# Performance work log

Measured on AMD Instinct MI355X. Metric: run time of the kernel, lower is better.

The kernel has to match this reference:

```python
import jax, jax.numpy as jnp
import numpy as np

B, S, D_IN, D_OUT, H = 1, 4096, 1024, 1024, 16
HD = D_OUT // H


def setup_inputs() -> dict:
    key = jax.random.key(0)
    ks = jax.random.split(key, 6)
    sc = 0.02
    return {
        "x": jax.random.normal(ks[0], (B, S, D_IN), dtype=jnp.float32),
        "Wq": jax.random.normal(ks[1], (D_IN, D_OUT), dtype=jnp.float32) * sc,
        "Wk": jax.random.normal(ks[2], (D_IN, D_OUT), dtype=jnp.float32) * sc,
        "Wv": jax.random.normal(ks[3], (D_IN, D_OUT), dtype=jnp.float32) * sc,
        "Wo": jax.random.normal(ks[4], (D_OUT, D_OUT), dtype=jnp.float32) * sc,
        "bo": jnp.zeros((D_OUT,), dtype=jnp.float32),
    }


def reference(x, Wq, Wk, Wv, Wo, bo):
    b, n, _ = x.shape
    # QKV projections (no bias), split into heads: [b, h, n, hd]
    def heads(w):
        return (x @ w).reshape(b, n, H, HD).transpose(0, 2, 1, 3)
    q, k, v = heads(Wq), heads(Wk), heads(Wv)
    # scores [b, h, n, n], causal mask, scaled softmax (dropout p=0 -> identity)
    scores = jnp.einsum("bhqd,bhkd->bhqk", q, k)
    causal = jnp.tril(jnp.ones((n, n), dtype=bool))
    scores = jnp.where(causal, scores, -jnp.inf)
    attn = jax.nn.softmax(scores / jnp.sqrt(jnp.float32(HD)), axis=-1)
    ctx = jnp.einsum("bhqk,bhkd->bhqd", attn, v)
    ctx = ctx.transpose(0, 2, 1, 3).reshape(b, n, D_OUT)
    return ctx @ Wo + bo
```

## Files before the change

kernel.cpp:

```cpp
#include <hip/hip_runtime.h>
#include <hip/hip_bf16.h>
#include <stdint.h>


typedef __bf16 bf16;
typedef __bf16 bf16x4 __attribute__((ext_vector_type(4)));
typedef __bf16 bf16x8 __attribute__((ext_vector_type(8)));
typedef float  f32x4  __attribute__((ext_vector_type(4)));

#define MFMA32(a, b, c) __builtin_amdgcn_mfma_f32_16x16x32_bf16((a), (b), (c), 0, 0, 0)

static constexpr int S_LEN  = 4096;
static constexpr int DMODEL = 1024;
static constexpr int HDIM   = 64;
static constexpr int LDQK   = 2048;

#define GLOAD_LDS16(g, l)                                                      \
  __builtin_amdgcn_global_load_lds((__attribute__((address_space(1))) void*)(g), \
                                   (__attribute__((address_space(3))) void*)(l), 16, 0, 0)

__global__ __launch_bounds__(256) void preprocess(const float* __restrict__ x,
                                                  const float* __restrict__ Wq,
                                                  const float* __restrict__ Wk,
                                                  const float* __restrict__ Wv,
                                                  const float* __restrict__ Wo,
                                                  bf16* __restrict__ xb,
                                                  bf16* __restrict__ Wt,
                                                  bf16* __restrict__ Wot) {
  __shared__ float tile[64][65];
  const int t = threadIdx.x, b = blockIdx.x;
  if (b < 1024) {
#pragma unroll
    for (int i = 0; i < 4; i++) {
      int idx = b * 1024 + i * 256 + t;
      float4 v = ((const float4*)x)[idx];
      bf16x4 o;
      o[0] = (bf16)v.x; o[1] = (bf16)v.y; o[2] = (bf16)v.z; o[3] = (bf16)v.w;
      ((bf16x4*)xb)[idx] = o;
    }
    return;
  }
  const int id = b - 1024;
  const int wsel = id >> 8;
  const int t2 = id & 255;
  const int kb = (t2 & 15) * 64, nb = (t2 >> 4) * 64;
  const float* src = (wsel == 0) ? Wq : (wsel == 1) ? Wk : (wsel == 2) ? Wv : Wo;
  bf16* dst = (wsel < 3) ? (Wt + (size_t)wsel * 1024 * 1024) : Wot;
#pragma unroll
  for (int i = 0; i < 16; i++) {
    int idx = t + i * 256;
    int r = idx >> 6, c = idx & 63;
    tile[r][c] = src[(size_t)(kb + r) * 1024 + nb + c];
  }
  __syncthreads();
#pragma unroll
  for (int i = 0; i < 16; i++) {
    int idx = t + i * 256;
    int cc = idx >> 6, rr = idx & 63;
    dst[(size_t)(nb + cc) * 1024 + kb + rr] = (bf16)tile[rr][cc];
  }
}

__global__ __launch_bounds__(256) void gemm_qkv(const bf16* __restrict__ A,
                                                const bf16* __restrict__ Bt,
                                                bf16* __restrict__ QK,
                                                bf16* __restrict__ Vt) {
  __shared__ bf16 lsA[128 * 32];
  __shared__ bf16 lsB[128 * 32];
  const int tid = threadIdx.x, w = tid >> 6, lane = tid & 63;
  const int l15 = lane & 15, quad = lane >> 4;
  const int m0 = blockIdx.x * 128, n0 = blockIdx.y * 128;
  const int wm = (w >> 1) * 64, wn = (w & 1) * 64;
  const int rowA = lane >> 2;
  const int colk = (lane & 3) * 8;

  f32x4 acc[4][4] = {};

  for (int k0 = 0; k0 < 1024; k0 += 32) {
    __syncthreads();
#pragma unroll
    for (int i = 0; i < 2; i++) {
      int s = w * 2 + i;
      const bf16* ga = A + (size_t)(m0 + s * 16 + rowA) * 1024 + k0 + colk;
      GLOAD_LDS16(ga, lsA + s * 512);
      const bf16* gb = Bt + (size_t)(n0 + s * 16 + rowA) * 1024 + k0 + colk;
      GLOAD_LDS16(gb, lsB + s * 512);
    }
    __syncthreads();

    bf16x8 af[4], bfr[4];
#pragma unroll
    for (int r = 0; r < 4; r++)
      af[r] = *(const bf16x8*)(lsA + (wm + r * 16 + l15) * 32 + quad * 8);
#pragma unroll
    for (int c = 0; c < 4; c++)
      bfr[c] = *(const bf16x8*)(lsB + (wn + c * 16 + l15) * 32 + quad * 8);
#pragma unroll
    for (int r = 0; r < 4; r++)
#pragma unroll
      for (int c = 0; c < 4; c++)
        acc[r][c] = MFMA32(af[r], bfr[c], acc[r][c]);
  }

  if (n0 < 2048) {
#pragma unroll
    for (int r = 0; r < 4; r++) {
#pragma unroll
      for (int c = 0; c < 4; c++) {
        int col = n0 + wn + c * 16 + l15;
        float scale = (col < 1024) ? 0.18033688f : 1.0f;
#pragma unroll
        for (int e = 0; e < 4; e++) {
          int row = m0 + wm + r * 16 + quad * 4 + e;
          QK[(size_t)row * LDQK + col] = (bf16)(acc[r][c][e] * scale);
        }
      }
    }
  } else {
#pragma unroll
    for (int r = 0; r < 4; r++) {
#pragma unroll
      for (int c = 0; c < 4; c++) {
        int vcol = (n0 - 2048) + wn + c * 16 + l15;
        int row0 = m0 + wm + r * 16 + quad * 4;
        bf16x4 pk;
#pragma unroll
        for (int e = 0; e < 4; e++) pk[e] = (bf16)acc[r][c][e];
        *(bf16x4*)(Vt + (size_t)vcol * S_LEN + row0) = pk;
      }
    }
  }
}

__global__ __launch_bounds__(256, 2) void flash_attn(const bf16* __restrict__ QK,
                                                     const bf16* __restrict__ Vt,
                                                     bf16* __restrict__ Ctx) {
  __shared__ float Obuf[4][16][68];
  __shared__ float Lbuf[4][4][64];
  const int tid = threadIdx.x, w = tid >> 6, lane = tid & 63;
  const int l15 = lane & 15, quad = lane >> 4;
  const int i = blockIdx.x;
  const int head = (i & 7) + 8 * ((i >> 3) & 1);
  const int qt_raw = i >> 4;
  const int qb = (qt_raw < 32) ? qt_raw : (95 - qt_raw);
  const int hq = head * HDIM;
  const int krow0 = w * 32 + ((l15 >> 2) << 3) + (l15 & 3);

  const int T = (qb >> 1) + 1;

  bf16x8 qf[4][2];
#pragma unroll
  for (int qg = 0; qg < 4; qg++)
#pragma unroll
    for (int kk = 0; kk < 2; kk++)
      qf[qg][kk] = *(const bf16x8*)(QK + (size_t)(qb * 64 + qg * 16 + l15) * LDQK +
                                    hq + kk * 32 + quad * 8);

  f32x4 oacc[4][4] = {};
  float lsum[4] = {0.f, 0.f, 0.f, 0.f};

  auto load_k = [&](int j, bf16x8 (&kf)[2][2]) {
#pragma unroll
    for (int c = 0; c < 2; c++)
#pragma unroll
      for (int kk = 0; kk < 2; kk++)
        kf[c][kk] = *(const bf16x8*)(QK + (size_t)(j * 128 + krow0 + 4 * c) * LDQK +
                                     DMODEL + hq + kk * 32 + quad * 8);
  };
  auto load_v = [&](int j, bf16x8 (&vf)[4]) {
#pragma unroll
    for (int dg = 0; dg < 4; dg++)
      vf[dg] = *(const bf16x8*)(Vt + (size_t)(hq + dg * 16 + l15) * S_LEN +
                                j * 128 + w * 32 + quad * 8);
  };
  auto compute = [&](int j, bf16x8 (&kf)[2][2], bf16x8 (&vf)[4]) {
    f32x4 sacc[2][4] = {};
#pragma unroll
    for (int kk = 0; kk < 2; kk++)
#pragma unroll
      for (int c = 0; c < 2; c++)
#pragma unroll
        for (int qg = 0; qg < 4; qg++)
          sacc[c][qg] = MFMA32(kf[c][kk], qf[qg][kk], sacc[c][qg]);

    bf16x8 pfr[4];
    if (j == T - 1) {
      const int kb0 = j * 128 + w * 32 + quad * 8;
#pragma unroll
      for (int qg = 0; qg < 4; qg++) {
        const int qrow = qb * 64 + qg * 16 + l15;
        bf16x8 pb;
#pragma unroll
        for (int c = 0; c < 2; c++)
#pragma unroll
          for (int e = 0; e < 4; e++) {
            float s = sacc[c][qg][e];
            if (kb0 + 4 * c + e > qrow) s = -1e30f;
            float pv = __builtin_amdgcn_exp2f(s);
            lsum[qg] += pv;
            pb[c * 4 + e] = (bf16)pv;
          }
        pfr[qg] = pb;
      }
    } else {
#pragma unroll
      for (int qg = 0; qg < 4; qg++) {
        bf16x8 pb;
#pragma unroll
        for (int c = 0; c < 2; c++)
#pragma unroll
          for (int e = 0; e < 4; e++) {
            float pv = __builtin_amdgcn_exp2f(sacc[c][qg][e]);
            lsum[qg] += pv;
            pb[c * 4 + e] = (bf16)pv;
          }
        pfr[qg] = pb;
      }
    }

#pragma unroll
    for (int qg = 0; qg < 4; qg++)
#pragma unroll
      for (int dg = 0; dg < 4; dg++)
        oacc[qg][dg] = MFMA32(pfr[qg], vf[dg], oacc[qg][dg]);
  };

  bf16x8 kfA[2][2], vfA[4], kfB[2][2], vfB[4];
  load_k(0, kfA); load_v(0, vfA);
  for (int j = 0; j < T; j += 2) {
    if (j + 1 < T) { load_k(j + 1, kfB); load_v(j + 1, vfB); }
    compute(j, kfA, vfA);
    if (j + 2 < T) { load_k(j + 2, kfA); load_v(j + 2, vfA); }
    if (j + 1 < T) compute(j + 1, kfB, vfB);
  }

#pragma unroll
  for (int qg = 0; qg < 4; qg++)
    Lbuf[w][quad][qg * 16 + l15] = lsum[qg];

  const int row = tid >> 4;
  const int col = (tid & 15) * 4;
  for (int qg = 0; qg < 4; qg++) {
#pragma unroll
    for (int dg = 0; dg < 4; dg++)
#pragma unroll
      for (int e = 0; e < 4; e++)
        Obuf[w][quad * 4 + e][dg * 16 + l15] = oacc[qg][dg][e];
    __syncthreads();
    f32x4 os = {};
#pragma unroll
    for (int ww = 0; ww < 4; ww++)
      os += *(const f32x4*)&Obuf[ww][row][col];
    float lr = 0.f;
#pragma unroll
    for (int ww = 0; ww < 4; ww++)
#pragma unroll
      for (int qq = 0; qq < 4; qq++)
        lr += Lbuf[ww][qq][qg * 16 + row];
    const float linv = 1.f / lr;
    bf16x4 ob;
#pragma unroll
    for (int e2 = 0; e2 < 4; e2++) ob[e2] = (bf16)(os[e2] * linv);
    *(bf16x4*)(Ctx + (size_t)(qb * 64 + qg * 16 + row) * DMODEL + hq + col) = ob;
    __syncthreads();
  }
}

__global__ __launch_bounds__(256) void gemm_out(const bf16* __restrict__ A,
                                                const bf16* __restrict__ Bt,
                                                float* __restrict__ C,
                                                const float* __restrict__ bias) {
  __shared__ bf16 lsA[64 * 32];
  __shared__ bf16 lsB[128 * 32];
  const int tid = threadIdx.x, w = tid >> 6, lane = tid & 63;
  const int l15 = lane & 15, quad = lane >> 4;
  const int m0 = blockIdx.x * 64, n0 = blockIdx.y * 128;
  const int wm = (w >> 1) * 32, wn = (w & 1) * 64;
  const int rowA = lane >> 2;
  const int colk = (lane & 3) * 8;

  f32x4 acc[2][4] = {};

  for (int k0 = 0; k0 < 1024; k0 += 32) {
    __syncthreads();
#pragma unroll
    for (int i = 0; i < 3; i++) {
      int s = w * 3 + i;
      if (s < 4) {
        const bf16* ga = A + (size_t)(m0 + s * 16 + rowA) * 1024 + k0 + colk;
        GLOAD_LDS16(ga, lsA + s * 512);
      } else {
        const bf16* gb = Bt + (size_t)(n0 + (s - 4) * 16 + rowA) * 1024 + k0 + colk;
        GLOAD_LDS16(gb, lsB + (s - 4) * 512);
      }
    }
    __syncthreads();

    bf16x8 af[2], bfr[4];
#pragma unroll
    for (int r = 0; r < 2; r++)
      af[r] = *(const bf16x8*)(lsA + (wm + r * 16 + l15) * 32 + quad * 8);
#pragma unroll
    for (int c = 0; c < 4; c++)
      bfr[c] = *(const bf16x8*)(lsB + (wn + c * 16 + l15) * 32 + quad * 8);
#pragma unroll
    for (int r = 0; r < 2; r++)
#pragma unroll
      for (int c = 0; c < 4; c++)
        acc[r][c] = MFMA32(af[r], bfr[c], acc[r][c]);
  }

#pragma unroll
  for (int r = 0; r < 2; r++) {
#pragma unroll
    for (int c = 0; c < 4; c++) {
      int col = n0 + wn + c * 16 + l15;
#pragma unroll
      for (int e = 0; e < 4; e++) {
        int row = m0 + wm + r * 16 + quad * 4 + e;
        C[(size_t)row * 1024 + col] = acc[r][c][e] + bias[col];
      }
    }
  }
}

extern "C" void kernel_launch(void* const* d_in, const int* in_sizes, int n_in,
                              void* d_out, int out_size, void* d_ws, size_t ws_size,
                              hipStream_t stream) {
  const float* x  = (const float*)d_in[0];
  const float* Wq = (const float*)d_in[1];
  const float* Wk = (const float*)d_in[2];
  const float* Wv = (const float*)d_in[3];
  const float* Wo = (const float*)d_in[4];
  const float* bo = (const float*)d_in[5];

  char* ws = (char*)d_ws;
  bf16* xb  = (bf16*)(ws);
  bf16* Wt  = (bf16*)(ws + (8u  << 20));
  bf16* Wot = (bf16*)(ws + (14u << 20));
  bf16* QK  = (bf16*)(ws + (16u << 20));
  bf16* Vt  = (bf16*)(ws + (32u << 20));
  bf16* Ctx = (bf16*)(ws + (40u << 20));

  preprocess<<<2048, 256, 0, stream>>>(x, Wq, Wk, Wv, Wo, xb, Wt, Wot);
  gemm_qkv<<<dim3(32, 24), 256, 0, stream>>>(xb, Wt, QK, Vt);
  flash_attn<<<1024, 256, 0, stream>>>(QK, Vt, Ctx);
  gemm_out<<<dim3(64, 8), 256, 0, stream>>>(Ctx, Wot, (float*)d_out, bo);
}
```

Before: 204.4 us.

## Split flash attention warps into 2x2 query/key halves with 64-key tiles

Reorganises the flash-attention block so the four waves form a 2x2 grid over query halves and key halves, with 64-row key tiles instead of 128. Each wave holds fewer accumulators, which lets occupancy rise to three blocks per SIMD. The wave whose only work is the fully masked diagonal quarter now skips it. Blocks are launched in descending order of query tile for longest-first scheduling, and V is no longer double-buffered, which exposes more V-load latency.

After: 268.8 us. +31.5%, slower.

```diff
diff --git a/kernel.cpp b/kernel.cpp
--- a/kernel.cpp
+++ b/kernel.cpp
@@ -132,63 +132,64 @@
   }
 }
 
-__global__ __launch_bounds__(256, 2) void flash_attn(const bf16* __restrict__ QK,
+__global__ __launch_bounds__(256, 3) void flash_attn(const bf16* __restrict__ QK,
                                                      const bf16* __restrict__ Vt,
                                                      bf16* __restrict__ Ctx) {
   __shared__ float Obuf[4][16][68];
-  __shared__ float Lbuf[4][4][64];
+  __shared__ float Lbuf[4][4][32];
   const int tid = threadIdx.x, w = tid >> 6, lane = tid & 63;
   const int l15 = lane & 15, quad = lane >> 4;
   const int i = blockIdx.x;
   const int head = (i & 7) + 8 * ((i >> 3) & 1);
-  const int qt_raw = i >> 4;
-  const int qb = (qt_raw < 32) ? qt_raw : (95 - qt_raw);
+  const int qb = 63 - (i >> 4);
   const int hq = head * HDIM;
-  const int krow0 = w * 32 + ((l15 >> 2) << 3) + (l15 & 3);
-
-  const int T = (qb >> 1) + 1;
-
-  bf16x8 qf[4][2];
-#pragma unroll
-  for (int qg = 0; qg < 4; qg++)
+  const int qhalf = w >> 1, khalf = w & 1;
+  const int q0 = qb * 64 + qhalf * 32;
+  const int krow0 = khalf * 32 + ((l15 >> 2) << 3) + (l15 & 3);
+  const int T = qb + 1;
+  const bool dead_diag = (khalf == 1) && (qhalf == 0);
+
+  bf16x8 qf[2][2];
+#pragma unroll
+  for (int qg = 0; qg < 2; qg++)
 #pragma unroll
     for (int kk = 0; kk < 2; kk++)
-      qf[qg][kk] = *(const bf16x8*)(QK + (size_t)(qb * 64 + qg * 16 + l15) * LDQK +
+      qf[qg][kk] = *(const bf16x8*)(QK + (size_t)(q0 + qg * 16 + l15) * LDQK +
                                     hq + kk * 32 + quad * 8);
 
-  f32x4 oacc[4][4] = {};
-  float lsum[4] = {0.f, 0.f, 0.f, 0.f};
+  f32x4 oacc[2][4] = {};
+  float lsum[2] = {0.f, 0.f};
 
   auto load_k = [&](int j, bf16x8 (&kf)[2][2]) {
 #pragma unroll
     for (int c = 0; c < 2; c++)
 #pragma unroll
       for (int kk = 0; kk < 2; kk++)
-        kf[c][kk] = *(const bf16x8*)(QK + (size_t)(j * 128 + krow0 + 4 * c) * LDQK +
+        kf[c][kk] = *(const bf16x8*)(QK + (size_t)(j * 64 + krow0 + 4 * c) * LDQK +
                                      DMODEL + hq + kk * 32 + quad * 8);
   };
   auto load_v = [&](int j, bf16x8 (&vf)[4]) {
 #pragma unroll
     for (int dg = 0; dg < 4; dg++)
       vf[dg] = *(const bf16x8*)(Vt + (size_t)(hq + dg * 16 + l15) * S_LEN +
-                                j * 128 + w * 32 + quad * 8);
+                                j * 64 + khalf * 32 + quad * 8);
   };
   auto compute = [&](int j, bf16x8 (&kf)[2][2], bf16x8 (&vf)[4]) {
-    f32x4 sacc[2][4] = {};
+    f32x4 sacc[2][2] = {};
 #pragma unroll
     for (int kk = 0; kk < 2; kk++)
 #pragma unroll
       for (int c = 0; c < 2; c++)
 #pragma unroll
-        for (int qg = 0; qg < 4; qg++)
+        for (int qg = 0; qg < 2; qg++)
           sacc[c][qg] = MFMA32(kf[c][kk], qf[qg][kk], sacc[c][qg]);
 
-    bf16x8 pfr[4];
+    bf16x8 pfr[2];
     if (j == T - 1) {
-      const int kb0 = j * 128 + w * 32 + quad * 8;
-#pragma unroll
-      for (int qg = 0; qg < 4; qg++) {
-        const int qrow = qb * 64 + qg * 16 + l15;
+      const int kb0 = j * 64 + khalf * 32 + quad * 8;
+#pragma unroll
+      for (int qg = 0; qg < 2; qg++) {
+        const int qrow = q0 + qg * 16 + l15;
         bf16x8 pb;
 #pragma unroll
         for (int c = 0; c < 2; c++)
@@ -204,7 +205,7 @@
       }
     } else {
 #pragma unroll
-      for (int qg = 0; qg < 4; qg++) {
+      for (int qg = 0; qg < 2; qg++) {
         bf16x8 pb;
 #pragma unroll
         for (int c = 0; c < 2; c++)
@@ -219,49 +220,70 @@
     }
 
 #pragma unroll
-    for (int qg = 0; qg < 4; qg++)
+    for (int qg = 0; qg < 2; qg++)
 #pragma unroll
       for (int dg = 0; dg < 4; dg++)
         oacc[qg][dg] = MFMA32(pfr[qg], vf[dg], oacc[qg][dg]);
   };
 
-  bf16x8 kfA[2][2], vfA[4], kfB[2][2], vfB[4];
-  load_k(0, kfA); load_v(0, vfA);
+  bf16x8 kfA[2][2], kfB[2][2], vf[4];
+  load_k(0, kfA);
   for (int j = 0; j < T; j += 2) {
-    if (j + 1 < T) { load_k(j + 1, kfB); load_v(j + 1, vfB); }
-    compute(j, kfA, vfA);
-    if (j + 2 < T) { load_k(j + 2, kfA); load_v(j + 2, vfA); }
-    if (j + 1 < T) compute(j + 1, kfB, vfB);
-  }
-
-#pragma unroll
-  for (int qg = 0; qg < 4; qg++)
+    const bool skip0 = dead_diag && (j == T - 1);
+    if (!skip0) load_v(j, vf);
+    if (j + 1 < T) load_k(j + 1, kfB);
+    if (!skip0) compute(j, kfA, vf);
+    if (j + 1 < T) {
+      const bool skip1 = dead_diag && (j + 1 == T - 1);
+      if (!skip1) load_v(j + 1, vf);
+      if (j + 2 < T) load_k(j + 2, kfA);
+      if (!skip1) compute(j + 1, kfB, vf);
+    }
+  }
+
+#pragma unroll
+  for (int qg = 0; qg < 2; qg++)
     Lbuf[w][quad][qg * 16 + l15] = lsum[qg];
 
   const int row = tid >> 4;
   const int col = (tid & 15) * 4;
-  for (int qg = 0; qg < 4; qg++) {
+  for (int cp = 0; cp < 2; cp++) {
 #pragma unroll
     for (int dg = 0; dg < 4; dg++)
 #pragma unroll
       for (int e = 0; e < 4; e++)
-        Obuf[w][quad * 4 + e][dg * 16 + l15] = oacc[qg][dg][e];
-    __syncthreads();
-    f32x4 os = {};
-#pragma unroll
-    for (int ww = 0; ww < 4; ww++)
-      os += *(const f32x4*)&Obuf[ww][row][col];
-    float lr = 0.f;
-#pragma unroll
-    for (int ww = 0; ww < 4; ww++)
+        Obuf[w][quad * 4 + e][dg * 16 + l15] = oacc[cp][dg][e];
+    __syncthreads();
+    f32x4 os0 = *(const f32x4*)&Obuf[0][row][col];
+    os0 += *(const f32x4*)&Obuf[1][row][col];
+    float lr0 = 0.f;
+#pragma unroll
+    for (int ww = 0; ww < 2; ww++)
 #pragma unroll
       for (int qq = 0; qq < 4; qq++)
-        lr += Lbuf[ww][qq][qg * 16 + row];
-    const float linv = 1.f / lr;
-    bf16x4 ob;
-#pragma unroll
-    for (int e2 = 0; e2 < 4; e2++) ob[e2] = (bf16)(os[e2] * linv);
-    *(bf16x4*)(Ctx + (size_t)(qb * 64 + qg * 16 + row) * DMODEL + hq + col) = ob;
+        lr0 += Lbuf[ww][qq][cp * 16 + row];
+    {
+      const float linv = 1.f / lr0;
+      bf16x4 ob;
+#pragma unroll
+      for (int e2 = 0; e2 < 4; e2++) ob[e2] = (bf16)(os0[e2] * linv);
+      *(bf16x4*)(Ctx + (size_t)(qb * 64 + cp * 16 + row) * DMODEL + hq + col) = ob;
+    }
+    f32x4 os1 = *(const f32x4*)&Obuf[2][row][col];
+    os1 += *(const f32x4*)&Obuf[3][row][col];
+    float lr1 = 0.f;
+#pragma unroll
+    for (int ww = 2; ww < 4; ww++)
+#pragma unroll
+      for (int qq = 0; qq < 4; qq++)
+        lr1 += Lbuf[ww][qq][cp * 16 + row];
+    {
+      const float linv = 1.f / lr1;
+      bf16x4 ob;
+#pragma unroll
+      for (int e2 = 0; e2 < 4; e2++) ob[e2] = (bf16)(os1[e2] * linv);
+      *(bf16x4*)(Ctx + (size_t)(qb * 64 + 32 + cp * 16 + row) * DMODEL + hq + col) = ob;
+    }
     __syncthreads();
   }
 }
```

## Halve flash-attention query tile to 32 rows and double grid with occupancy 4

Applied to the files above, without the earlier changes.

Shrinks each attention block from 64 to 32 query rows, doubling the grid to 2048 blocks and raising launch bounds to 4 blocks per CU. Blocks are ordered from longest to shortest causal extent, and warps whose key slice lies entirely past the diagonal skip their last tile. MFMA sections are wrapped in s_setprio to favour compute waves. The aim is better load balance and latency hiding, at the cost of less Q reuse per K/V load and more total K/V traffic.

Measured after the change: 372.7 us. +82.4%, slower.

```diff
diff --git a/kernel.cpp b/kernel.cpp
--- a/kernel.cpp
+++ b/kernel.cpp
@@ -132,32 +132,32 @@
   }
 }
 
-__global__ __launch_bounds__(256, 2) void flash_attn(const bf16* __restrict__ QK,
+__global__ __launch_bounds__(256, 4) void flash_attn(const bf16* __restrict__ QK,
                                                      const bf16* __restrict__ Vt,
                                                      bf16* __restrict__ Ctx) {
   __shared__ float Obuf[4][16][68];
-  __shared__ float Lbuf[4][4][64];
+  __shared__ float Lbuf[4][4][32];
   const int tid = threadIdx.x, w = tid >> 6, lane = tid & 63;
   const int l15 = lane & 15, quad = lane >> 4;
   const int i = blockIdx.x;
   const int head = (i & 7) + 8 * ((i >> 3) & 1);
-  const int qt_raw = i >> 4;
-  const int qb = (qt_raw < 32) ? qt_raw : (95 - qt_raw);
+  const int qb = 127 - (i >> 4);
   const int hq = head * HDIM;
+  const int q0 = qb * 32;
   const int krow0 = w * 32 + ((l15 >> 2) << 3) + (l15 & 3);
-
-  const int T = (qb >> 1) + 1;
-
-  bf16x8 qf[4][2];
-#pragma unroll
-  for (int qg = 0; qg < 4; qg++)
+  const int T = (qb >> 2) + 1;
+  const int Tw = T - ((w > (qb & 3)) ? 1 : 0);
+
+  bf16x8 qf[2][2];
+#pragma unroll
+  for (int qg = 0; qg < 2; qg++)
 #pragma unroll
     for (int kk = 0; kk < 2; kk++)
-      qf[qg][kk] = *(const bf16x8*)(QK + (size_t)(qb * 64 + qg * 16 + l15) * LDQK +
+      qf[qg][kk] = *(const bf16x8*)(QK + (size_t)(q0 + qg * 16 + l15) * LDQK +
                                     hq + kk * 32 + quad * 8);
 
-  f32x4 oacc[4][4] = {};
-  float lsum[4] = {0.f, 0.f, 0.f, 0.f};
+  f32x4 oacc[2][4] = {};
+  float lsum[2] = {0.f, 0.f};
 
   auto load_k = [&](int j, bf16x8 (&kf)[2][2]) {
 #pragma unroll
@@ -174,21 +174,22 @@
                                 j * 128 + w * 32 + quad * 8);
   };
   auto compute = [&](int j, bf16x8 (&kf)[2][2], bf16x8 (&vf)[4]) {
-    f32x4 sacc[2][4] = {};
+    __builtin_amdgcn_s_setprio(1);
+    f32x4 sacc[2][2] = {};
 #pragma unroll
     for (int kk = 0; kk < 2; kk++)
 #pragma unroll
       for (int c = 0; c < 2; c++)
 #pragma unroll
-        for (int qg = 0; qg < 4; qg++)
+        for (int qg = 0; qg < 2; qg++)
           sacc[c][qg] = MFMA32(kf[c][kk], qf[qg][kk], sacc[c][qg]);
 
-    bf16x8 pfr[4];
+    bf16x8 pfr[2];
     if (j == T - 1) {
       const int kb0 = j * 128 + w * 32 + quad * 8;
 #pragma unroll
-      for (int qg = 0; qg < 4; qg++) {
-        const int qrow = qb * 64 + qg * 16 + l15;
+      for (int qg = 0; qg < 2; qg++) {
+        const int qrow = q0 + qg * 16 + l15;
         bf16x8 pb;
 #pragma unroll
         for (int c = 0; c < 2; c++)
@@ -204,7 +205,7 @@
       }
     } else {
 #pragma unroll
-      for (int qg = 0; qg < 4; qg++) {
+      for (int qg = 0; qg < 2; qg++) {
         bf16x8 pb;
 #pragma unroll
         for (int c = 0; c < 2; c++)
@@ -219,33 +220,36 @@
     }
 
 #pragma unroll
-    for (int qg = 0; qg < 4; qg++)
+    for (int qg = 0; qg < 2; qg++)
 #pragma unroll
       for (int dg = 0; dg < 4; dg++)
         oacc[qg][dg] = MFMA32(pfr[qg], vf[dg], oacc[qg][dg]);
+    __builtin_amdgcn_s_setprio(0);
   };
 
-  bf16x8 kfA[2][2], vfA[4], kfB[2][2], vfB[4];
-  load_k(0, kfA); load_v(0, vfA);
-  for (int j = 0; j < T; j += 2) {
-    if (j + 1 < T) { load_k(j + 1, kfB); load_v(j + 1, vfB); }
-    compute(j, kfA, vfA);
-    if (j + 2 < T) { load_k(j + 2, kfA); load_v(j + 2, vfA); }
-    if (j + 1 < T) compute(j + 1, kfB, vfB);
-  }
-
-#pragma unroll
-  for (int qg = 0; qg < 4; qg++)
+  bf16x8 kfA[2][2], kfB[2][2], vfA[4], vfB[4];
+  if (Tw > 0) {
+    load_k(0, kfA); load_v(0, vfA);
+    for (int j = 0; j < Tw; j += 2) {
+      if (j + 1 < Tw) { load_k(j + 1, kfB); load_v(j + 1, vfB); }
+      compute(j, kfA, vfA);
+      if (j + 2 < Tw) { load_k(j + 2, kfA); load_v(j + 2, vfA); }
+      if (j + 1 < Tw) compute(j + 1, kfB, vfB);
+    }
+  }
+
+#pragma unroll
+  for (int qg = 0; qg < 2; qg++)
     Lbuf[w][quad][qg * 16 + l15] = lsum[qg];
 
   const int row = tid >> 4;
   const int col = (tid & 15) * 4;
-  for (int qg = 0; qg < 4; qg++) {
+  for (int cp = 0; cp < 2; cp++) {
 #pragma unroll
     for (int dg = 0; dg < 4; dg++)
 #pragma unroll
       for (int e = 0; e < 4; e++)
-        Obuf[w][quad * 4 + e][dg * 16 + l15] = oacc[qg][dg][e];
+        Obuf[w][quad * 4 + e][dg * 16 + l15] = oacc[cp][dg][e];
     __syncthreads();
     f32x4 os = {};
 #pragma unroll
@@ -256,12 +260,12 @@
     for (int ww = 0; ww < 4; ww++)
 #pragma unroll
       for (int qq = 0; qq < 4; qq++)
-        lr += Lbuf[ww][qq][qg * 16 + row];
+        lr += Lbuf[ww][qq][cp * 16 + row];
     const float linv = 1.f / lr;
     bf16x4 ob;
 #pragma unroll
     for (int e2 = 0; e2 < 4; e2++) ob[e2] = (bf16)(os[e2] * linv);
-    *(bf16x4*)(Ctx + (size_t)(qb * 64 + qg * 16 + row) * DMODEL + hq + col) = ob;
+    *(bf16x4*)(Ctx + (size_t)(q0 + cp * 16 + row) * DMODEL + hq + col) = ob;
     __syncthreads();
   }
 }
@@ -344,6 +348,6 @@
 
   preprocess<<<2048, 256, 0, stream>>>(x, Wq, Wk, Wv, Wo, xb, Wt, Wot);
   gemm_qkv<<<dim3(32, 24), 256, 0, stream>>>(xb, Wt, QK, Vt);
-  flash_attn<<<1024, 256, 0, stream>>>(QK, Vt, Ctx);
+  flash_attn<<<2048, 256, 0, stream>>>(QK, Vt, Ctx);
   gemm_out<<<dim3(64, 8), 256, 0, stream>>>(Ctx, Wot, (float*)d_out, bo);
 }
```
